# Kernel optimization log

Measured on AMD Instinct MI355X. Metric: run time of the kernel, lower is better.

## Reference

```python
import jax, jax.numpy as jnp
import numpy as np

N_NODES = 50000
N_EDGES = 800000
HID = 96

def setup_inputs() -> dict:
    key = jax.random.key(0)
    ks = jax.random.split(key, 12)
    s = 1.0 / np.sqrt(HID)
    return {
        "x_feat": jax.random.normal(ks[0], (N_NODES, HID), jnp.float32),
        "bases": jax.random.normal(ks[1], (N_EDGES, HID), jnp.float32) * 0.1,
        "W_pre": jax.random.normal(ks[2], (HID, HID), jnp.float32) * s,
        "b_pre": jax.random.normal(ks[3], (HID,), jnp.float32) * s,
        "W1": jax.random.normal(ks[4], (HID, HID), jnp.float32) * s,
        "b1": jax.random.normal(ks[5], (HID,), jnp.float32) * s,
        "W2": jax.random.normal(ks[6], (HID, HID), jnp.float32) * s,
        "b2": jax.random.normal(ks[7], (HID,), jnp.float32) * s,
        "src": jax.random.randint(ks[8], (N_EDGES,), 0, N_NODES, jnp.int32),
        "dst": jax.random.randint(ks[9], (N_EDGES,), 0, N_NODES, jnp.int32),
    }

def _gelu(x):
    return jax.nn.gelu(x, approximate=False)  # torch nn.GELU default = erf

def reference(x_feat, bases, W_pre, b_pre, W1, b1, W2, b2, src, dst):
    n = x_feat.shape[0]
    # pre_ffn: Linear + GELU on node features
    h = _gelu(x_feat @ W_pre + b_pre)                      # [N, H]
    # update_all(u_mul_e('x','v'), sum): gather src feats, weight by edge bases, scatter-add to dst
    msg = h[src] * bases                                   # [E, H]
    aggr = jax.ops.segment_sum(msg, dst, num_segments=n)   # [N, H]
    # dropout is identity in eval mode (rate=0)
    x = x_feat + aggr                                      # residual 1
    y = _gelu(_gelu(x @ W1 + b1) @ W2 + b2)                # ffn (no batch norm)
    return x + y                                           # residual 2
```

## Files before the change

### kernel.cpp

```cpp
#include <hip/hip_runtime.h>

#define NODES 50000
#define EDGES 800000
#define H 96
#define CAP 64

typedef float floatx4 __attribute__((ext_vector_type(4)));
typedef unsigned short ushort8 __attribute__((ext_vector_type(8)));
typedef __bf16 bf16x8 __attribute__((ext_vector_type(8)));

static __device__ __forceinline__ unsigned short f2b(float f) {
    unsigned int u = __float_as_uint(f);
    u = u + 0x7fffu + ((u >> 16) & 1u);
    return (unsigned short)(u >> 16);
}
static __device__ __forceinline__ float b2f(unsigned short u) {
    return __uint_as_float(((unsigned int)u) << 16);
}
static __device__ __forceinline__ float gelu_erf(float x) {
    return 0.5f * x * (1.0f + erff(x * 0.70710678118654752f));
}
static __device__ __forceinline__ bf16x8 pack_bf8(const float* a) {
    union { ushort8 u; bf16x8 v; } r;
    #pragma unroll
    for (int j = 0; j < 8; ++j) r.u[j] = f2b(a[j]);
    return r.v;
}

__global__ __launch_bounds__(256) void gemm96_pre(
    const float* __restrict__ A,
    const float* __restrict__ W,
    const float* __restrict__ bias,
    unsigned short* __restrict__ outp,
    int* __restrict__ cursor,
    int nStrips)
{
    const int g = blockIdx.x * 256 + threadIdx.x;
    if (g < NODES) cursor[g] = g * CAP;

    __shared__ unsigned short Wt[96][104];
    const int tid = threadIdx.x;
    #pragma unroll
    for (int j = 0; j < 36; ++j) {
        const int f = tid + 256 * j;
        const int k = f / 96, n = f - k * 96;
        Wt[n][k] = f2b(W[f]);
    }
    __syncthreads();

    const int lane = tid & 63;
    const int quad = lane >> 4;
    const int l16  = lane & 15;

    bf16x8 Bf[3][6];
    float  bv[6];
    #pragma unroll
    for (int ks = 0; ks < 3; ++ks)
        #pragma unroll
        for (int nt = 0; nt < 6; ++nt)
            Bf[ks][nt] = *(const bf16x8*)(&Wt[nt * 16 + l16][ks * 32 + quad * 8]);
    #pragma unroll
    for (int nt = 0; nt < 6; ++nt) bv[nt] = bias[nt * 16 + l16];

    const int gwave  = (blockIdx.x * 256 + tid) >> 6;
    const int nWaves = (gridDim.x * 256) >> 6;

    for (int strip = gwave; strip < nStrips; strip += nWaves) {
        const int row0 = strip * 16;
        const float* Ap = A + (size_t)(row0 + l16) * H + quad * 8;

        bf16x8 Af[3];
        #pragma unroll
        for (int ks = 0; ks < 3; ++ks) {
            float tmp[8];
            const floatx4 a0 = *(const floatx4*)(Ap + ks * 32);
            const floatx4 a1 = *(const floatx4*)(Ap + ks * 32 + 4);
            #pragma unroll
            for (int j = 0; j < 4; ++j) { tmp[j] = a0[j]; tmp[4 + j] = a1[j]; }
            Af[ks] = pack_bf8(tmp);
        }

        floatx4 acc[6];
        #pragma unroll
        for (int nt = 0; nt < 6; ++nt) acc[nt] = (floatx4){0.f, 0.f, 0.f, 0.f};
        #pragma unroll
        for (int ks = 0; ks < 3; ++ks)
            #pragma unroll
            for (int nt = 0; nt < 6; ++nt)
                acc[nt] = __builtin_amdgcn_mfma_f32_16x16x32_bf16(Af[ks], Bf[ks][nt], acc[nt], 0, 0, 0);

        #pragma unroll
        for (int nt = 0; nt < 6; ++nt) {
            const int col = nt * 16 + l16;
            #pragma unroll
            for (int r = 0; r < 4; ++r) {
                const int row = row0 + quad * 4 + r;
                outp[(size_t)row * H + col] = f2b(gelu_erf(acc[nt][r] + bv[nt]));
            }
        }
    }
}

__global__ __launch_bounds__(256) void build_csr2(
    const int* __restrict__ dst, const int* __restrict__ src,
    int* __restrict__ cursor, int2* __restrict__ csr)
{
    const int e = blockIdx.x * 256 + threadIdx.x;
    if (e < EDGES) {
        const int d = dst[e];
        const int p = atomicAdd(&cursor[d], 1);
        if (p < d * CAP + CAP) {
            int2 es; es.x = e; es.y = src[e];
            csr[p] = es;
        }
    }
}

__global__ __launch_bounds__(256, 8) void gather_nodes(
    const unsigned short* __restrict__ h,
    const float* __restrict__ bases,
    const int2* __restrict__ csr,
    const int* __restrict__ cursor,
    const float* __restrict__ x_feat,
    float* __restrict__ xb)
{
    const int t = blockIdx.x * 256 + threadIdx.x;
    const int n = t / 12;
    if (n >= NODES) return;
    const int seg = t - n * 12;
    const int so8 = seg * 8;
    const int i0 = n * CAP;
    const int i1 = min(cursor[n], i0 + CAP);

    floatx4 acc0 = (floatx4){0.f, 0.f, 0.f, 0.f};
    floatx4 acc1 = (floatx4){0.f, 0.f, 0.f, 0.f};

    int i = i0;
    for (; i + 1 < i1; i += 2) {
        const int2 ea = csr[i];
        const int2 eb = csr[i + 1];
        const size_t eoa = (size_t)ea.x * H + so8;
        const size_t eob = (size_t)eb.x * H + so8;
        const floatx4 ba0 = *(const floatx4*)(bases + eoa);
        const floatx4 ba1 = *(const floatx4*)(bases + eoa + 4);
        const ushort8 hva = *(const ushort8*)(h + (size_t)ea.y * H + so8);
        const floatx4 bb0 = *(const floatx4*)(bases + eob);
        const floatx4 bb1 = *(const floatx4*)(bases + eob + 4);
        const ushort8 hvb = *(const ushort8*)(h + (size_t)eb.y * H + so8);
        #pragma unroll
        for (int j = 0; j < 4; ++j) {
            acc0[j] = fmaf(ba0[j], b2f(hva[j]),     acc0[j]);
            acc1[j] = fmaf(ba1[j], b2f(hva[4 + j]), acc1[j]);
        }
        #pragma unroll
        for (int j = 0; j < 4; ++j) {
            acc0[j] = fmaf(bb0[j], b2f(hvb[j]),     acc0[j]);
            acc1[j] = fmaf(bb1[j], b2f(hvb[4 + j]), acc1[j]);
        }
    }
    if (i < i1) {
        const int2 ea = csr[i];
        const size_t eoa = (size_t)ea.x * H + so8;
        const floatx4 ba0 = *(const floatx4*)(bases + eoa);
        const floatx4 ba1 = *(const floatx4*)(bases + eoa + 4);
        const ushort8 hva = *(const ushort8*)(h + (size_t)ea.y * H + so8);
        #pragma unroll
        for (int j = 0; j < 4; ++j) {
            acc0[j] = fmaf(ba0[j], b2f(hva[j]),     acc0[j]);
            acc1[j] = fmaf(ba1[j], b2f(hva[4 + j]), acc1[j]);
        }
    }

    const size_t no = (size_t)n * H + so8;
    const floatx4 x0 = *(const floatx4*)(x_feat + no);
    const floatx4 x1 = *(const floatx4*)(x_feat + no + 4);
    #pragma unroll
    for (int j = 0; j < 4; ++j) { acc0[j] += x0[j]; acc1[j] += x1[j]; }
    *(floatx4*)(xb + no)     = acc0;
    *(floatx4*)(xb + no + 4) = acc1;
}

__global__ __launch_bounds__(256) void ffn_dual(
    const float* __restrict__ A,
    const float* __restrict__ W1, const float* __restrict__ b1,
    const float* __restrict__ W2, const float* __restrict__ b2,
    float* __restrict__ outp,
    int nStrips)
{
    __shared__ unsigned short Wt1[96][104];
    __shared__ unsigned short Wt2[96][104];
    __shared__ unsigned short St[4][16][112];

    const int tid = threadIdx.x;
    #pragma unroll
    for (int j = 0; j < 36; ++j) {
        const int f = tid + 256 * j;
        const int k = f / 96, n = f - k * 96;
        Wt1[n][k] = f2b(W1[f]);
        Wt2[n][k] = f2b(W2[f]);
    }
    __syncthreads();

    const int lane = tid & 63;
    const int quad = lane >> 4;
    const int l16  = lane & 15;
    const int w    = tid >> 6;

    float bv1[6], bv2[6];
    #pragma unroll
    for (int nt = 0; nt < 6; ++nt) {
        bv1[nt] = b1[nt * 16 + l16];
        bv2[nt] = b2[nt * 16 + l16];
    }

    const int wsw = quad << 3;
    const int rsw = (l16 >> 2) << 3;

    const int gwave  = (blockIdx.x * 256 + tid) >> 6;
    const int nWaves = (gridDim.x * 256) >> 6;

    for (int strip = gwave; strip < nStrips; strip += nWaves) {
        const int row0 = strip * 16;
        const float* Ap = A + (size_t)(row0 + l16) * H + quad * 8;

        bf16x8 Af[3];
        #pragma unroll
        for (int ks = 0; ks < 3; ++ks) {
            float tmp[8];
            const floatx4 a0 = *(const floatx4*)(Ap + ks * 32);
            const floatx4 a1 = *(const floatx4*)(Ap + ks * 32 + 4);
            #pragma unroll
            for (int j = 0; j < 4; ++j) { tmp[j] = a0[j]; tmp[4 + j] = a1[j]; }
            Af[ks] = pack_bf8(tmp);
        }
        floatx4 facc[6];
        #pragma unroll
        for (int nt = 0; nt < 6; ++nt) facc[nt] = (floatx4){0.f, 0.f, 0.f, 0.f};
        #pragma unroll
        for (int ks = 0; ks < 3; ++ks)
            #pragma unroll
            for (int nt = 0; nt < 6; ++nt) {
                const bf16x8 Bf1 = *(const bf16x8*)(&Wt1[nt * 16 + l16][ks * 32 + quad * 8]);
                facc[nt] = __builtin_amdgcn_mfma_f32_16x16x32_bf16(Af[ks], Bf1, facc[nt], 0, 0, 0);
            }

        #pragma unroll
        for (int nt = 0; nt < 6; ++nt)
            #pragma unroll
            for (int r = 0; r < 4; ++r)
                St[w][quad * 4 + r][(nt * 16 + l16) ^ wsw] =
                    f2b(gelu_erf(facc[nt][r] + bv1[nt]));
        bf16x8 Tf[3];
        #pragma unroll
        for (int ks = 0; ks < 3; ++ks)
            Tf[ks] = *(const bf16x8*)(&St[w][l16][(ks * 32 + quad * 8) ^ rsw]);

        #pragma unroll
        for (int nt = 0; nt < 6; ++nt) facc[nt] = (floatx4){0.f, 0.f, 0.f, 0.f};
        #pragma unroll
        for (int ks = 0; ks < 3; ++ks)
            #pragma unroll
            for (int nt = 0; nt < 6; ++nt) {
                const bf16x8 Bf2 = *(const bf16x8*)(&Wt2[nt * 16 + l16][ks * 32 + quad * 8]);
                facc[nt] = __builtin_amdgcn_mfma_f32_16x16x32_bf16(Tf[ks], Bf2, facc[nt], 0, 0, 0);
            }
        #pragma unroll
        for (int nt = 0; nt < 6; ++nt) {
            const int col = nt * 16 + l16;
            #pragma unroll
            for (int r = 0; r < 4; ++r) {
                const int row = row0 + quad * 4 + r;
                const size_t o = (size_t)row * H + col;
                outp[o] = A[o] + gelu_erf(facc[nt][r] + bv2[nt]);
            }
        }
    }
}

extern "C" void kernel_launch(void* const* d_in, const int* in_sizes, int n_in,
                              void* d_out, int out_size, void* d_ws, size_t ws_size,
                              hipStream_t stream)
{
    const float* x_feat = (const float*)d_in[0];
    const float* bases  = (const float*)d_in[1];
    const float* W_pre  = (const float*)d_in[2];
    const float* b_pre  = (const float*)d_in[3];
    const float* W1     = (const float*)d_in[4];
    const float* b1     = (const float*)d_in[5];
    const float* W2     = (const float*)d_in[6];
    const float* b2     = (const float*)d_in[7];
    const int* src = (const int*)d_in[8];
    const int* dst = (const int*)d_in[9];

    char* ws = (char*)d_ws;
    int*            cursor = (int*)(ws);
    int2*           csr2   = (int2*)(ws + 1048576);
    unsigned short* h_bf   = (unsigned short*)(ws + 27262976);
    float*          xb     = (float*)(ws + 37748736);
    float*          out    = (float*)d_out;

    const int nStrips = NODES / 16;

    gemm96_pre<<<512, 256, 0, stream>>>(x_feat, W_pre, b_pre, h_bf, cursor, nStrips);
    build_csr2<<<(EDGES + 255) / 256, 256, 0, stream>>>(dst, src, cursor, csr2);
    gather_nodes<<<(NODES * 12 + 255) / 256, 256, 0, stream>>>(
        h_bf, bases, csr2, cursor, x_feat, xb);
    ffn_dual<<<512, 256, 0, stream>>>(xb, W1, b1, W2, b2, out, nStrips);
}
```

Before: 535.1 us.

## Fuse CSR bucket scatter into pre-GEMM launch and use nontemporal gather loads

Merges the edge-bucketing kernel into the pre-FFN GEMM launch by giving extra blocks the scatter work, so the two independent phases can run concurrently on the GPU. Per-node counters are now zeroed with a memset and the kernel stores counts instead of absolute cursors. The gather kernel reads csr, bases and x_feat with nontemporal loads to keep streaming data from evicting the reused h rows in cache. The cost is an extra memset launch, and the GEMM and scatter blocks now compete for the same resources.

```diff
diff --git a/kernel.cpp b/kernel.cpp
--- a/kernel.cpp
+++ b/kernel.cpp
@@ -27,19 +27,33 @@
     return r.v;
 }
 
-__global__ __launch_bounds__(256) void gemm96_pre(
+__global__ __launch_bounds__(256) void pre_scatter(
     const float* __restrict__ A,
     const float* __restrict__ W,
     const float* __restrict__ bias,
     unsigned short* __restrict__ outp,
-    int* __restrict__ cursor,
-    int nStrips)
+    const int* __restrict__ dst,
+    const int* __restrict__ src,
+    int* __restrict__ count,
+    int2* __restrict__ csr,
+    int nStrips, int nGemmBlocks)
 {
-    const int g = blockIdx.x * 256 + threadIdx.x;
-    if (g < NODES) cursor[g] = g * CAP;
-
     __shared__ unsigned short Wt[96][104];
     const int tid = threadIdx.x;
+
+    if (blockIdx.x >= nGemmBlocks) {
+        const int e = (blockIdx.x - nGemmBlocks) * 256 + tid;
+        if (e < EDGES) {
+            const int d = dst[e];
+            const int c = atomicAdd(&count[d], 1);
+            if (c < CAP) {
+                int2 es; es.x = e; es.y = src[e];
+                csr[d * CAP + c] = es;
+            }
+        }
+        return;
+    }
+
     #pragma unroll
     for (int j = 0; j < 36; ++j) {
         const int f = tid + 256 * j;
@@ -63,7 +77,7 @@
     for (int nt = 0; nt < 6; ++nt) bv[nt] = bias[nt * 16 + l16];
 
     const int gwave  = (blockIdx.x * 256 + tid) >> 6;
-    const int nWaves = (gridDim.x * 256) >> 6;
+    const int nWaves = (nGemmBlocks * 256) >> 6;
 
     for (int strip = gwave; strip < nStrips; strip += nWaves) {
         const int row0 = strip * 16;
@@ -101,26 +115,11 @@
     }
 }
 
-__global__ __launch_bounds__(256) void build_csr2(
-    const int* __restrict__ dst, const int* __restrict__ src,
-    int* __restrict__ cursor, int2* __restrict__ csr)
-{
-    const int e = blockIdx.x * 256 + threadIdx.x;
-    if (e < EDGES) {
-        const int d = dst[e];
-        const int p = atomicAdd(&cursor[d], 1);
-        if (p < d * CAP + CAP) {
-            int2 es; es.x = e; es.y = src[e];
-            csr[p] = es;
-        }
-    }
-}
-
 __global__ __launch_bounds__(256, 8) void gather_nodes(
     const unsigned short* __restrict__ h,
     const float* __restrict__ bases,
     const int2* __restrict__ csr,
-    const int* __restrict__ cursor,
+    const int* __restrict__ count,
     const float* __restrict__ x_feat,
     float* __restrict__ xb)
 {
@@ -130,23 +129,27 @@
     const int seg = t - n * 12;
     const int so8 = seg * 8;
     const int i0 = n * CAP;
-    const int i1 = min(cursor[n], i0 + CAP);
+    const int i1 = i0 + min(count[n], CAP);
 
     floatx4 acc0 = (floatx4){0.f, 0.f, 0.f, 0.f};
     floatx4 acc1 = (floatx4){0.f, 0.f, 0.f, 0.f};
 
     int i = i0;
     for (; i + 1 < i1; i += 2) {
-        const int2 ea = csr[i];
-        const int2 eb = csr[i + 1];
-        const size_t eoa = (size_t)ea.x * H + so8;
-        const size_t eob = (size_t)eb.x * H + so8;
-        const floatx4 ba0 = *(const floatx4*)(bases + eoa);
-        const floatx4 ba1 = *(const floatx4*)(bases + eoa + 4);
-        const ushort8 hva = *(const ushort8*)(h + (size_t)ea.y * H + so8);
-        const floatx4 bb0 = *(const floatx4*)(bases + eob);
-        const floatx4 bb1 = *(const floatx4*)(bases + eob + 4);
-        const ushort8 hvb = *(const ushort8*)(h + (size_t)eb.y * H + so8);
+        const unsigned long long pa =
+            __builtin_nontemporal_load((const unsigned long long*)&csr[i]);
+        const unsigned long long pb =
+            __builtin_nontemporal_load((const unsigned long long*)&csr[i + 1]);
+        const int ea = (int)pa, sa = (int)(pa >> 32);
+        const int eb = (int)pb, sb = (int)(pb >> 32);
+        const float* bpa = bases + (size_t)ea * H + so8;
+        const float* bpb = bases + (size_t)eb * H + so8;
+        const floatx4 ba0 = __builtin_nontemporal_load((const floatx4*)(bpa));
+        const floatx4 ba1 = __builtin_nontemporal_load((const floatx4*)(bpa + 4));
+        const ushort8 hva = *(const ushort8*)(h + (size_t)sa * H + so8);
+        const floatx4 bb0 = __builtin_nontemporal_load((const floatx4*)(bpb));
+        const floatx4 bb1 = __builtin_nontemporal_load((const floatx4*)(bpb + 4));
+        const ushort8 hvb = *(const ushort8*)(h + (size_t)sb * H + so8);
         #pragma unroll
         for (int j = 0; j < 4; ++j) {
             acc0[j] = fmaf(ba0[j], b2f(hva[j]),     acc0[j]);
@@ -159,11 +162,13 @@
         }
     }
     if (i < i1) {
-        const int2 ea = csr[i];
-        const size_t eoa = (size_t)ea.x * H + so8;
-        const floatx4 ba0 = *(const floatx4*)(bases + eoa);
-        const floatx4 ba1 = *(const floatx4*)(bases + eoa + 4);
-        const ushort8 hva = *(const ushort8*)(h + (size_t)ea.y * H + so8);
+        const unsigned long long pa =
+            __builtin_nontemporal_load((const unsigned long long*)&csr[i]);
+        const int ea = (int)pa, sa = (int)(pa >> 32);
+        const float* bpa = bases + (size_t)ea * H + so8;
+        const floatx4 ba0 = __builtin_nontemporal_load((const floatx4*)(bpa));
+        const floatx4 ba1 = __builtin_nontemporal_load((const floatx4*)(bpa + 4));
+        const ushort8 hva = *(const ushort8*)(h + (size_t)sa * H + so8);
         #pragma unroll
         for (int j = 0; j < 4; ++j) {
             acc0[j] = fmaf(ba0[j], b2f(hva[j]),     acc0[j]);
@@ -172,8 +177,8 @@
     }
 
     const size_t no = (size_t)n * H + so8;
-    const floatx4 x0 = *(const floatx4*)(x_feat + no);
-    const floatx4 x1 = *(const floatx4*)(x_feat + no + 4);
+    const floatx4 x0 = __builtin_nontemporal_load((const floatx4*)(x_feat + no));
+    const floatx4 x1 = __builtin_nontemporal_load((const floatx4*)(x_feat + no + 4));
     #pragma unroll
     for (int j = 0; j < 4; ++j) { acc0[j] += x0[j]; acc1[j] += x1[j]; }
     *(floatx4*)(xb + no)     = acc0;
@@ -293,17 +298,20 @@
     const int* dst = (const int*)d_in[9];
 
     char* ws = (char*)d_ws;
-    int*            cursor = (int*)(ws);
+    int*            count  = (int*)(ws);
     int2*           csr2   = (int2*)(ws + 1048576);
     unsigned short* h_bf   = (unsigned short*)(ws + 27262976);
     float*          xb     = (float*)(ws + 37748736);
     float*          out    = (float*)d_out;
 
-    const int nStrips = NODES / 16;
-
-    gemm96_pre<<<512, 256, 0, stream>>>(x_feat, W_pre, b_pre, h_bf, cursor, nStrips);
-    build_csr2<<<(EDGES + 255) / 256, 256, 0, stream>>>(dst, src, cursor, csr2);
+    const int nStrips     = NODES / 16;
+    const int nGemmBlocks = 512;
+    const int nScatBlocks = (EDGES + 255) / 256;
+
+    hipMemsetAsync(count, 0, NODES * sizeof(int), stream);
+    pre_scatter<<<nGemmBlocks + nScatBlocks, 256, 0, stream>>>(
+        x_feat, W_pre, b_pre, h_bf, dst, src, count, csr2, nStrips, nGemmBlocks);
     gather_nodes<<<(NODES * 12 + 255) / 256, 256, 0, stream>>>(
-        h_bf, bases, csr2, cursor, x_feat, xb);
+        h_bf, bases, csr2, count, x_feat, xb);
     ffn_dual<<<512, 256, 0, stream>>>(xb, W1, b1, W2, b2, out, nStrips);
 }
```

After: 536.0 us. No clear change (+0.2%).
